# Kernel optimization log

Measured on AMD Instinct MI355X. Metric: run time of the kernel, lower is better.

Reference implementation:

```python
import jax, jax.numpy as jnp
import numpy as np

KERNEL = 3
DILATIONS = (2, 3)
NUM_HEADS = 8


def _unfold_windows(t, k, dil):
    # t: [B, C, H, W] -> [B, C, k*k, H, W], same layout as nn.Unfold(k, dil, pad=dil*(k-1)//2)
    B, C, H, W = t.shape
    pad = dil * (k - 1) // 2
    tp = jnp.pad(t, ((0, 0), (0, 0), (pad, pad), (pad, pad)))
    ws = [tp[:, :, i * dil:i * dil + H, j * dil:j * dil + W]
          for i in range(k) for j in range(k)]
    return jnp.stack(ws, axis=2)


def _dilate_attention(q, k_, v, kernel, dil, head_dim):
    # q,k_,v: [B, d, H, W]
    B, d, H, W = q.shape
    nh = d // head_dim
    scale = head_dim ** (-0.5)
    qh = q.reshape(B, nh, head_dim, H, W)
    kw = _unfold_windows(k_, kernel, dil).reshape(B, nh, head_dim, kernel * kernel, H, W)
    vw = _unfold_windows(v, kernel, dil).reshape(B, nh, head_dim, kernel * kernel, H, W)
    attn = jax.nn.softmax(jnp.einsum('bndhw,bndkhw->bnkhw', qh, kw) * scale, axis=2)
    out = jnp.einsum('bnkhw,bndkhw->bndhw', attn, vw)  # [B, nh, hd, H, W]
    return out.transpose(0, 3, 4, 1, 2).reshape(B, H, W, d)


def setup_inputs() -> dict:
    key = jax.random.key(0)
    k1, k2, k3, k4 = jax.random.split(key, 4)
    B, H, W, C = 4, 128, 128, 256
    x = jax.random.normal(k1, (B, H, W, C), dtype=jnp.float32)
    Wqkv = jax.random.normal(k2, (3 * C, C), dtype=jnp.float32) * (C ** -0.5)
    Wproj = jax.random.normal(k3, (C, C), dtype=jnp.float32) * (C ** -0.5)
    bproj = jnp.zeros((C,), dtype=jnp.float32)
    return {"x": x, "Wqkv": Wqkv, "Wproj": Wproj, "bproj": bproj}


def reference(x, Wqkv, Wproj, bproj):
    B, H, W, C = x.shape
    nd = len(DILATIONS)
    head_dim = C // NUM_HEADS
    # 1x1 conv qkv (no bias), then split into 3 and nd dilation groups
    qkv = jnp.einsum('bhwc,oc->bohw', x, Wqkv).reshape(B, 3, nd, C // nd, H, W)
    outs = []
    for i, dil in enumerate(DILATIONS):
        q, k_, v = qkv[:, 0, i], qkv[:, 1, i], qkv[:, 2, i]
        outs.append(_dilate_attention(q, k_, v, KERNEL, dil, head_dim))
    xo = jnp.concatenate(outs, axis=-1)  # [B, H, W, C], dilation-group-major channels
    return jnp.einsum('bhwc,oc->bhwo', xo, Wproj) + bproj
```

## Files before the change

kernel.cpp:

```cpp
#include <hip/hip_runtime.h>
#include <stdint.h>


typedef __attribute__((ext_vector_type(8))) short bf16x8;
typedef __attribute__((ext_vector_type(4))) float f32x4;
typedef __attribute__((ext_vector_type(2))) float f32x2;

__device__ __forceinline__ f32x2 up2(unsigned u) {
  union { unsigned u; float f; } a, b;
  a.u = u << 16;
  b.u = u & 0xffff0000u;
  return (f32x2){a.f, b.f};
}
__device__ __forceinline__ unsigned short f2bf(float f) {
  union { float f; unsigned u; } x; x.f = f;
  unsigned r = x.u + 0x7fffu + ((x.u >> 16) & 1u);
  return (unsigned short)(r >> 16);
}
__device__ __forceinline__ unsigned pk2bf(float a, float b) {
  return (unsigned)f2bf(a) | ((unsigned)f2bf(b) << 16);
}
__device__ __forceinline__ unsigned cvtpk(float a, float b) {
  unsigned r;
  asm("v_cvt_pk_bf16_f32 %0, %1, %2" : "=v"(r) : "v"(a), "v"(b));
  return r;
}

__global__ __launch_bounds__(256) void cvt_w_both(
    const float* __restrict__ wqkv, const float* __restrict__ wproj,
    unsigned short* __restrict__ dst) {
  const int i = (blockIdx.x * 256 + threadIdx.x) * 8;
  const float* src = (i < 196608) ? (wqkv + i) : (wproj + (i - 196608));
  const float4* s = (const float4*)src;
  float4 a = s[0], b = s[1];
  uint4 o;
  o.x = pk2bf(a.x, a.y); o.y = pk2bf(a.z, a.w);
  o.z = pk2bf(b.x, b.y); o.w = pk2bf(b.z, b.w);
  *(uint4*)(dst + i) = o;
}

#define BARX()                                                \
  do {                                                        \
    asm volatile("s_waitcnt lgkmcnt(0)" ::: "memory");        \
    __builtin_amdgcn_s_barrier();                             \
    __builtin_amdgcn_sched_barrier(0);                        \
  } while (0)
#define WAITVM(n)                                             \
  do {                                                        \
    asm volatile("s_waitcnt vmcnt(" #n ")" ::: "memory");     \
    __builtin_amdgcn_sched_barrier(0);                        \
  } while (0)

template <int OUTF32, int AF32>
__global__ __launch_bounds__(256) void gemm_bt(
    const void* __restrict__ Ap, const unsigned short* __restrict__ B,
    void* __restrict__ Cout, const float* __restrict__ bias,
    int N, int NT) {
  __shared__ __align__(16) unsigned short lds[24576];

  const int tid  = threadIdx.x;
  const int lane = tid & 63;
  const int wv   = tid >> 6;
  const int wr   = wv >> 1;
  const int wc   = wv & 1;

  const int nwg = gridDim.x;
  const int q8  = nwg >> 3;
  const int nid = (blockIdx.x & 7) * q8 + (blockIdx.x >> 3);
  const int n0  = (nid % NT) * 128;
  const int m0  = (nid / NT) * 128;

  const float* Af          = (const float*)Ap;
  const unsigned short* Ab = (const unsigned short*)Ap;

  const int stg_rowB = wv * 16 + (lane >> 2);
  const int stg_kB   = ((lane & 3) ^ ((lane >> 3) & 3)) * 8;
  const unsigned short* Bg   = B  + (size_t)(n0 + stg_rowB) * 256 + stg_kB;
  const unsigned short* Ag16 = Ab + (size_t)(m0 + stg_rowB) * 256 + stg_kB;

  const int stg_rowA32 = wv * 8 + (lane >> 3);
  const int stg_kA32   = ((lane & 7) ^ (lane >> 3)) * 4;
  const float* Ag32 = Af + (size_t)(m0 + stg_rowA32) * 256 + stg_kA32;

  f32x4 acc[4][4];
#pragma unroll
  for (int i = 0; i < 4; ++i)
#pragma unroll
    for (int j = 0; j < 4; ++j) acc[i][j] = (f32x4){0.f, 0.f, 0.f, 0.f};

  const int a_r = lane & 15;

#define STAGE16(buf, kt)                                                       \
  do {                                                                         \
    const unsigned short* Asrc = Ag16 + (kt) * 32;                             \
    const unsigned short* Bsrc = Bg + (kt) * 32;                               \
    _Pragma("unroll")                                                          \
    for (int it = 0; it < 2; ++it) {                                           \
      __builtin_amdgcn_global_load_lds(                                        \
          (const __attribute__((address_space(1))) void*)(Asrc + (size_t)it * 64 * 256), \
          (__attribute__((address_space(3))) void*)&lds[(buf) * 8192 + it * 2048 + wv * 512], \
          16, 0, 0);                                                           \
      __builtin_amdgcn_global_load_lds(                                        \
          (const __attribute__((address_space(1))) void*)(Bsrc + (size_t)it * 64 * 256), \
          (__attribute__((address_space(3))) void*)&lds[(buf) * 8192 + 4096 + it * 2048 + wv * 512], \
          16, 0, 0);                                                           \
    }                                                                          \
  } while (0)

#define COMPUTE16(buf)                                                         \
  do {                                                                         \
    const int gsw = (((lane >> 4) ^ ((lane >> 1) & 3))) * 8;                   \
    bf16x8 af[4], bfr[4];                                                      \
    _Pragma("unroll")                                                          \
    for (int mi = 0; mi < 4; ++mi)                                             \
      af[mi] = *(const bf16x8*)&lds[(buf) * 8192 + (wr * 64 + mi * 16 + a_r) * 32 + gsw]; \
    _Pragma("unroll")                                                          \
    for (int ni = 0; ni < 4; ++ni)                                             \
      bfr[ni] = *(const bf16x8*)&lds[(buf) * 8192 + 4096 + (wc * 64 + ni * 16 + a_r) * 32 + gsw]; \
    _Pragma("unroll")                                                          \
    for (int mi = 0; mi < 4; ++mi)                                             \
      _Pragma("unroll")                                                        \
      for (int ni = 0; ni < 4; ++ni)                                           \
        acc[mi][ni] = __builtin_amdgcn_mfma_f32_16x16x32_bf16(                 \
            af[mi], bfr[ni], acc[mi][ni], 0, 0, 0);                            \
  } while (0)

#define STAGE32(buf, kt)                                                       \
  do {                                                                         \
    const float* Asrc = Ag32 + (kt) * 32;                                      \
    const unsigned short* Bsrc = Bg + (kt) * 32;                               \
    _Pragma("unroll")                                                          \
    for (int it = 0; it < 4; ++it)                                             \
      __builtin_amdgcn_global_load_lds(                                        \
          (const __attribute__((address_space(1))) void*)(Asrc + (size_t)it * 32 * 256), \
          (__attribute__((address_space(3))) void*)&lds[(buf) * 12288 + it * 2048 + wv * 512], \
          16, 0, 0);                                                           \
    _Pragma("unroll")                                                          \
    for (int it = 0; it < 2; ++it)                                             \
      __builtin_amdgcn_global_load_lds(                                        \
          (const __attribute__((address_space(1))) void*)(Bsrc + (size_t)it * 64 * 256), \
          (__attribute__((address_space(3))) void*)&lds[(buf) * 12288 + 8192 + it * 2048 + wv * 512], \
          16, 0, 0);                                                           \
  } while (0)

#define COMPUTE32(buf)                                                         \
  do {                                                                         \
    const int gswB = (((lane >> 4) ^ ((lane >> 1) & 3))) * 8;                  \
    const int sA0  = ((2 * (lane >> 4)) ^ (lane & 7)) * 4;                     \
    const int sA1  = (((2 * (lane >> 4)) ^ (lane & 7)) ^ 1) * 4;               \
    const float* Afl = (const float*)lds;                                      \
    bf16x8 af[4], bfr[4];                                                      \
    _Pragma("unroll")                                                          \
    for (int mi = 0; mi < 4; ++mi) {                                           \
      const int rb = (buf) * 6144 + (wr * 64 + mi * 16 + a_r) * 32;            \
      f32x4 lo = *(const f32x4*)&Afl[rb + sA0];                                \
      f32x4 hi = *(const f32x4*)&Afl[rb + sA1];                                \
      uint4 pk;                                                                \
      pk.x = cvtpk(lo.x, lo.y); pk.y = cvtpk(lo.z, lo.w);                      \
      pk.z = cvtpk(hi.x, hi.y); pk.w = cvtpk(hi.z, hi.w);                      \
      af[mi] = *(bf16x8*)&pk;                                                  \
    }                                                                          \
    _Pragma("unroll")                                                          \
    for (int ni = 0; ni < 4; ++ni)                                             \
      bfr[ni] = *(const bf16x8*)&lds[(buf) * 12288 + 8192 + (wc * 64 + ni * 16 + a_r) * 32 + gswB]; \
    _Pragma("unroll")                                                          \
    for (int mi = 0; mi < 4; ++mi)                                             \
      _Pragma("unroll")                                                        \
      for (int ni = 0; ni < 4; ++ni)                                           \
        acc[mi][ni] = __builtin_amdgcn_mfma_f32_16x16x32_bf16(                 \
            af[mi], bfr[ni], acc[mi][ni], 0, 0, 0);                            \
  } while (0)

  if constexpr (AF32) {
    STAGE32(0, 0);
    STAGE32(1, 1);
    WAITVM(6);  BARX();
    COMPUTE32(0); BARX();
    STAGE32(0, 2); WAITVM(6); BARX();
    COMPUTE32(1); BARX();
    STAGE32(1, 3); WAITVM(6); BARX();
    COMPUTE32(0); BARX();
    STAGE32(0, 4); WAITVM(6); BARX();
    COMPUTE32(1); BARX();
    STAGE32(1, 5); WAITVM(6); BARX();
    COMPUTE32(0); BARX();
    STAGE32(0, 6); WAITVM(6); BARX();
    COMPUTE32(1); BARX();
    STAGE32(1, 7); WAITVM(6); BARX();
    COMPUTE32(0); BARX();
    WAITVM(0);   BARX();
    COMPUTE32(1); BARX();
  } else {
    STAGE16(0, 0);
    STAGE16(1, 1);
    WAITVM(4); BARX();
    COMPUTE16(0); STAGE16(2, 2); WAITVM(4); BARX();
    COMPUTE16(1); STAGE16(0, 3); WAITVM(4); BARX();
    COMPUTE16(2); STAGE16(1, 4); WAITVM(4); BARX();
    COMPUTE16(0); STAGE16(2, 5); WAITVM(4); BARX();
    COMPUTE16(1); STAGE16(0, 6); WAITVM(4); BARX();
    COMPUTE16(2); STAGE16(1, 7); WAITVM(4); BARX();
    COMPUTE16(0); WAITVM(0);   BARX();
    COMPUTE16(1); BARX();
  }

  const int cl = wc * 64 + a_r;
  const int rl = wr * 64 + (lane >> 4) * 4;
  if (!OUTF32) {
    unsigned short* eb = &lds[0];
#pragma unroll
    for (int ni = 0; ni < 4; ++ni)
#pragma unroll
      for (int mi = 0; mi < 4; ++mi)
#pragma unroll
        for (int r = 0; r < 4; ++r)
          eb[(rl + mi * 16 + r) * 136 + cl + ni * 16] = f2bf(acc[mi][ni][r]);
    BARX();
    unsigned short* C = (unsigned short*)Cout;
#pragma unroll
    for (int p = 0; p < 8; ++p) {
      const int idx = p * 256 + tid;
      const int row = idx >> 4;
      const int seg = idx & 15;
      uint4 v = *(const uint4*)&eb[row * 136 + seg * 8];
      *(uint4*)&C[(size_t)(m0 + row) * N + n0 + seg * 8] = v;
    }
  } else {
    float* ef = (float*)&lds[0];
    float* C = (float*)Cout;
    float bv[4];
#pragma unroll
    for (int ni = 0; ni < 4; ++ni) bv[ni] = bias[n0 + wc * 64 + ni * 16 + a_r];
#pragma unroll
    for (int half = 0; half < 2; ++half) {
      if (wr == half) {
        const int rb = (lane >> 4) * 4;
#pragma unroll
        for (int ni = 0; ni < 4; ++ni)
#pragma unroll
          for (int mi = 0; mi < 4; ++mi)
#pragma unroll
            for (int r = 0; r < 4; ++r)
              ef[(rb + mi * 16 + r) * 132 + wc * 64 + ni * 16 + a_r] =
                  acc[mi][ni][r] + bv[ni];
      }
      BARX();
#pragma unroll
      for (int p = 0; p < 8; ++p) {
        const int idx = p * 256 + tid;
        const int row = idx >> 5;
        const int seg = idx & 31;
        f32x4 v = *(const f32x4*)&ef[row * 132 + seg * 4];
        *(f32x4*)&C[(size_t)(m0 + half * 64 + row) * N + n0 + seg * 4] = v;
      }
      BARX();
    }
  }
#undef STAGE16
#undef COMPUTE16
#undef STAGE32
#undef COMPUTE32
}

__global__ __launch_bounds__(512) void attn_kernel(
    const unsigned short* __restrict__ qkv, unsigned short* __restrict__ xo) {
  __shared__ __align__(16) unsigned short lds[4 * 485 * 8];

  const int nwg = gridDim.x;
  const int q8  = nwg >> 3;
  const int nid = (blockIdx.x & 7) * q8 + (blockIdx.x >> 3);
  const int combo = nid & 7;
  const int tw    = (nid >> 3) & 7;
  const int th    = (nid >> 6) & 7;
  const int b     = nid >> 9;
  const int d     = (combo >> 2) ? 3 : 2;
  const int choff = combo * 32;
  const int h0 = th * 16, w0 = tw * 16;
  const int t = threadIdx.x;

  const int splane = t & 3;
  const int t4     = t >> 2;
  const int schoff = choff + splane * 8;

#pragma unroll
  for (int it = 0; it < 4; ++it) {
    const int px = it * 128 + t4;
    const int r = px / 22, c = px % 22;
    const int gh = h0 - d + r;
    const int gw = w0 - d + c;
    const bool ok = ((unsigned)gh < 128u) && ((unsigned)gw < 128u);
    const int hcl = min(max(gh, 0), 127);
    const int wcl = min(max(gw, 0), 127);
    const int gp = (((b << 7) | hcl) << 7) | wcl;
    uint4 u = *(const uint4*)(qkv + (size_t)gp * 768 + 256 + schoff);
    if (!ok) u = make_uint4(0u, 0u, 0u, 0u);
    if (it < 3 || t < 400) *(uint4*)&lds[(splane * 485 + px) * 8] = u;
  }

  const int half = t & 1;
  const int ph = (t >> 1) >> 4, pw = (t >> 1) & 15;
  const int gp0 = (((b << 7) | (h0 + ph)) << 7) | (w0 + pw);
  const unsigned short* qp = qkv + (size_t)gp0 * 768 + choff + half * 16;
  uint4 uq0 = *(const uint4*)qp;
  uint4 uq1 = *(const uint4*)(qp + 8);
  f32x2 q2[8];
  {
    const f32x2 s2 = {0.17677669529663687f, 0.17677669529663687f};
    q2[0] = up2(uq0.x) * s2; q2[1] = up2(uq0.y) * s2;
    q2[2] = up2(uq0.z) * s2; q2[3] = up2(uq0.w) * s2;
    q2[4] = up2(uq1.x) * s2; q2[5] = up2(uq1.y) * s2;
    q2[6] = up2(uq1.z) * s2; q2[7] = up2(uq1.w) * s2;
  }
  __syncthreads();

  const int p0 = 2 * half, p1 = 2 * half + 1;
  float sc[9];
#pragma unroll
  for (int i = 0; i < 3; ++i) {
#pragma unroll
    for (int j = 0; j < 3; ++j) {
      const int lp = (ph + i * d) * 22 + (pw + j * d);
      const uint4 k0 = *(const uint4*)&lds[(p0 * 485 + lp) * 8];
      const uint4 k1 = *(const uint4*)&lds[(p1 * 485 + lp) * 8];
      f32x2 a = q2[0] * up2(k0.x);
      a += q2[1] * up2(k0.y); a += q2[2] * up2(k0.z); a += q2[3] * up2(k0.w);
      a += q2[4] * up2(k1.x); a += q2[5] * up2(k1.y);
      a += q2[6] * up2(k1.z); a += q2[7] * up2(k1.w);
      sc[i * 3 + j] = a.x + a.y;
    }
  }
#pragma unroll
  for (int k = 0; k < 9; ++k) sc[k] += __shfl_xor(sc[k], 1);

  float mx = sc[0];
#pragma unroll
  for (int k = 1; k < 9; ++k) mx = fmaxf(mx, sc[k]);
  float sum = 0.f;
#pragma unroll
  for (int k = 0; k < 9; ++k) { sc[k] = __expf(sc[k] - mx); sum += sc[k]; }
  const float inv = 1.f / sum;

  __syncthreads();
#pragma unroll
  for (int it = 0; it < 4; ++it) {
    const int px = it * 128 + t4;
    const int r = px / 22, c = px % 22;
    const int gh = h0 - d + r;
    const int gw = w0 - d + c;
    const bool ok = ((unsigned)gh < 128u) && ((unsigned)gw < 128u);
    const int hcl = min(max(gh, 0), 127);
    const int wcl = min(max(gw, 0), 127);
    const int gp = (((b << 7) | hcl) << 7) | wcl;
    uint4 u = *(const uint4*)(qkv + (size_t)gp * 768 + 512 + schoff);
    if (!ok) u = make_uint4(0u, 0u, 0u, 0u);
    if (it < 3 || t < 400) *(uint4*)&lds[(splane * 485 + px) * 8] = u;
  }
  __syncthreads();

  f32x2 o2[8];
#pragma unroll
  for (int k = 0; k < 8; ++k) o2[k] = (f32x2){0.f, 0.f};
#pragma unroll
  for (int i = 0; i < 3; ++i) {
#pragma unroll
    for (int j = 0; j < 3; ++j) {
      const int lp = (ph + i * d) * 22 + (pw + j * d);
      const uint4 v0 = *(const uint4*)&lds[(p0 * 485 + lp) * 8];
      const uint4 v1 = *(const uint4*)&lds[(p1 * 485 + lp) * 8];
      const float wv = sc[i * 3 + j] * inv;
      const f32x2 w2 = {wv, wv};
      o2[0] += w2 * up2(v0.x); o2[1] += w2 * up2(v0.y);
      o2[2] += w2 * up2(v0.z); o2[3] += w2 * up2(v0.w);
      o2[4] += w2 * up2(v1.x); o2[5] += w2 * up2(v1.y);
      o2[6] += w2 * up2(v1.z); o2[7] += w2 * up2(v1.w);
    }
  }

  unsigned short* op = xo + (size_t)gp0 * 256 + choff + half * 16;
  uint4 s0, s1;
  s0.x = pk2bf(o2[0].x, o2[0].y); s0.y = pk2bf(o2[1].x, o2[1].y);
  s0.z = pk2bf(o2[2].x, o2[2].y); s0.w = pk2bf(o2[3].x, o2[3].y);
  s1.x = pk2bf(o2[4].x, o2[4].y); s1.y = pk2bf(o2[5].x, o2[5].y);
  s1.z = pk2bf(o2[6].x, o2[6].y); s1.w = pk2bf(o2[7].x, o2[7].y);
  *(uint4*)op       = s0;
  *(uint4*)(op + 8) = s1;
}

extern "C" void kernel_launch(void* const* d_in, const int* in_sizes, int n_in,
                              void* d_out, int out_size, void* d_ws, size_t ws_size,
                              hipStream_t stream) {
  const float* x     = (const float*)d_in[0];
  const float* Wqkv  = (const float*)d_in[1];
  const float* Wproj = (const float*)d_in[2];
  const float* bproj = (const float*)d_in[3];

  const int M = 4 * 128 * 128;
  const int C = 256;

  unsigned short* qkvb   = (unsigned short*)d_ws;
  unsigned short* xob    = qkvb + (size_t)M * 3 * C;
  unsigned short* wqkvb  = xob + (size_t)M * C;
  unsigned short* wprojb = wqkvb + (size_t)3 * C * C;
  (void)wprojb;

  cvt_w_both<<<128, 256, 0, stream>>>(Wqkv, Wproj, wqkvb);

  gemm_bt<0, 1><<<(M / 128) * (3 * C / 128), 256, 0, stream>>>(
      (const void*)x, wqkvb, (void*)qkvb, nullptr, 3 * C, 3 * C / 128);

  attn_kernel<<<2048, 512, 0, stream>>>(qkvb, xob);

  gemm_bt<1, 0><<<(M / 128) * (C / 128), 256, 0, stream>>>(
      (const void*)xob, wqkvb + (size_t)3 * C * C, d_out, bproj, C, C / 128);
}
```

Measured before the change: 110.7 us.

## Specialize projection GEMM to full-width 128x256 tiles with 512 threads

Splits the templated GEMM into a QKV kernel and a dedicated projection kernel. Each projection workgroup now covers all 256 output columns for 128 rows with 8 waves, so every A tile is loaded once instead of twice, and the projection drops from three-stage to two-stage buffering. This is meant to cut redundant global loads of the attention output and halve the number of projection workgroups. The trade-off is fewer, larger blocks with higher LDS use per block, less overlap from the shallower pipeline, and an epilogue that writes the fp32 result in four quarter passes.

```diff
diff --git a/kernel.cpp b/kernel.cpp
--- a/kernel.cpp
+++ b/kernel.cpp
@@ -51,11 +51,9 @@
     __builtin_amdgcn_sched_barrier(0);                        \
   } while (0)
 
-template <int OUTF32, int AF32>
-__global__ __launch_bounds__(256) void gemm_bt(
-    const void* __restrict__ Ap, const unsigned short* __restrict__ B,
-    void* __restrict__ Cout, const float* __restrict__ bias,
-    int N, int NT) {
+__global__ __launch_bounds__(256) void gemm_qkv(
+    const float* __restrict__ Af, const unsigned short* __restrict__ B,
+    unsigned short* __restrict__ Cout, int N, int NT) {
   __shared__ __align__(16) unsigned short lds[24576];
 
   const int tid  = threadIdx.x;
@@ -70,13 +68,9 @@
   const int n0  = (nid % NT) * 128;
   const int m0  = (nid / NT) * 128;
 
-  const float* Af          = (const float*)Ap;
-  const unsigned short* Ab = (const unsigned short*)Ap;
-
   const int stg_rowB = wv * 16 + (lane >> 2);
   const int stg_kB   = ((lane & 3) ^ ((lane >> 3) & 3)) * 8;
-  const unsigned short* Bg   = B  + (size_t)(n0 + stg_rowB) * 256 + stg_kB;
-  const unsigned short* Ag16 = Ab + (size_t)(m0 + stg_rowB) * 256 + stg_kB;
+  const unsigned short* Bg = B + (size_t)(n0 + stg_rowB) * 256 + stg_kB;
 
   const int stg_rowA32 = wv * 8 + (lane >> 3);
   const int stg_kA32   = ((lane & 7) ^ (lane >> 3)) * 4;
@@ -89,41 +83,6 @@
     for (int j = 0; j < 4; ++j) acc[i][j] = (f32x4){0.f, 0.f, 0.f, 0.f};
 
   const int a_r = lane & 15;
-
-#define STAGE16(buf, kt)                                                       \
-  do {                                                                         \
-    const unsigned short* Asrc = Ag16 + (kt) * 32;                             \
-    const unsigned short* Bsrc = Bg + (kt) * 32;                               \
-    _Pragma("unroll")                                                          \
-    for (int it = 0; it < 2; ++it) {                                           \
-      __builtin_amdgcn_global_load_lds(                                        \
-          (const __attribute__((address_space(1))) void*)(Asrc + (size_t)it * 64 * 256), \
-          (__attribute__((address_space(3))) void*)&lds[(buf) * 8192 + it * 2048 + wv * 512], \
-          16, 0, 0);                                                           \
-      __builtin_amdgcn_global_load_lds(                                        \
-          (const __attribute__((address_space(1))) void*)(Bsrc + (size_t)it * 64 * 256), \
-          (__attribute__((address_space(3))) void*)&lds[(buf) * 8192 + 4096 + it * 2048 + wv * 512], \
-          16, 0, 0);                                                           \
-    }                                                                          \
-  } while (0)
-
-#define COMPUTE16(buf)                                                         \
-  do {                                                                         \
-    const int gsw = (((lane >> 4) ^ ((lane >> 1) & 3))) * 8;                   \
-    bf16x8 af[4], bfr[4];                                                      \
-    _Pragma("unroll")                                                          \
-    for (int mi = 0; mi < 4; ++mi)                                             \
-      af[mi] = *(const bf16x8*)&lds[(buf) * 8192 + (wr * 64 + mi * 16 + a_r) * 32 + gsw]; \
-    _Pragma("unroll")                                                          \
-    for (int ni = 0; ni < 4; ++ni)                                             \
-      bfr[ni] = *(const bf16x8*)&lds[(buf) * 8192 + 4096 + (wc * 64 + ni * 16 + a_r) * 32 + gsw]; \
-    _Pragma("unroll")                                                          \
-    for (int mi = 0; mi < 4; ++mi)                                             \
-      _Pragma("unroll")                                                        \
-      for (int ni = 0; ni < 4; ++ni)                                           \
-        acc[mi][ni] = __builtin_amdgcn_mfma_f32_16x16x32_bf16(                 \
-            af[mi], bfr[ni], acc[mi][ni], 0, 0, 0);                            \
-  } while (0)
 
 #define STAGE32(buf, kt)                                                       \
   do {                                                                         \
@@ -171,95 +130,160 @@
             af[mi], bfr[ni], acc[mi][ni], 0, 0, 0);                            \
   } while (0)
 
-  if constexpr (AF32) {
-    STAGE32(0, 0);
-    STAGE32(1, 1);
-    WAITVM(6);  BARX();
-    COMPUTE32(0); BARX();
-    STAGE32(0, 2); WAITVM(6); BARX();
-    COMPUTE32(1); BARX();
-    STAGE32(1, 3); WAITVM(6); BARX();
-    COMPUTE32(0); BARX();
-    STAGE32(0, 4); WAITVM(6); BARX();
-    COMPUTE32(1); BARX();
-    STAGE32(1, 5); WAITVM(6); BARX();
-    COMPUTE32(0); BARX();
-    STAGE32(0, 6); WAITVM(6); BARX();
-    COMPUTE32(1); BARX();
-    STAGE32(1, 7); WAITVM(6); BARX();
-    COMPUTE32(0); BARX();
-    WAITVM(0);   BARX();
-    COMPUTE32(1); BARX();
-  } else {
-    STAGE16(0, 0);
-    STAGE16(1, 1);
-    WAITVM(4); BARX();
-    COMPUTE16(0); STAGE16(2, 2); WAITVM(4); BARX();
-    COMPUTE16(1); STAGE16(0, 3); WAITVM(4); BARX();
-    COMPUTE16(2); STAGE16(1, 4); WAITVM(4); BARX();
-    COMPUTE16(0); STAGE16(2, 5); WAITVM(4); BARX();
-    COMPUTE16(1); STAGE16(0, 6); WAITVM(4); BARX();
-    COMPUTE16(2); STAGE16(1, 7); WAITVM(4); BARX();
-    COMPUTE16(0); WAITVM(0);   BARX();
-    COMPUTE16(1); BARX();
-  }
+  STAGE32(0, 0);
+  STAGE32(1, 1);
+  WAITVM(6);  BARX();
+  COMPUTE32(0); BARX();
+  STAGE32(0, 2); WAITVM(6); BARX();
+  COMPUTE32(1); BARX();
+  STAGE32(1, 3); WAITVM(6); BARX();
+  COMPUTE32(0); BARX();
+  STAGE32(0, 4); WAITVM(6); BARX();
+  COMPUTE32(1); BARX();
+  STAGE32(1, 5); WAITVM(6); BARX();
+  COMPUTE32(0); BARX();
+  STAGE32(0, 6); WAITVM(6); BARX();
+  COMPUTE32(1); BARX();
+  STAGE32(1, 7); WAITVM(6); BARX();
+  COMPUTE32(0); BARX();
+  WAITVM(0);   BARX();
+  COMPUTE32(1); BARX();
 
   const int cl = wc * 64 + a_r;
   const int rl = wr * 64 + (lane >> 4) * 4;
-  if (!OUTF32) {
-    unsigned short* eb = &lds[0];
-#pragma unroll
-    for (int ni = 0; ni < 4; ++ni)
-#pragma unroll
-      for (int mi = 0; mi < 4; ++mi)
-#pragma unroll
-        for (int r = 0; r < 4; ++r)
-          eb[(rl + mi * 16 + r) * 136 + cl + ni * 16] = f2bf(acc[mi][ni][r]);
-    BARX();
-    unsigned short* C = (unsigned short*)Cout;
-#pragma unroll
-    for (int p = 0; p < 8; ++p) {
-      const int idx = p * 256 + tid;
-      const int row = idx >> 4;
-      const int seg = idx & 15;
-      uint4 v = *(const uint4*)&eb[row * 136 + seg * 8];
-      *(uint4*)&C[(size_t)(m0 + row) * N + n0 + seg * 8] = v;
-    }
-  } else {
-    float* ef = (float*)&lds[0];
-    float* C = (float*)Cout;
-    float bv[4];
-#pragma unroll
-    for (int ni = 0; ni < 4; ++ni) bv[ni] = bias[n0 + wc * 64 + ni * 16 + a_r];
-#pragma unroll
-    for (int half = 0; half < 2; ++half) {
-      if (wr == half) {
-        const int rb = (lane >> 4) * 4;
-#pragma unroll
-        for (int ni = 0; ni < 4; ++ni)
-#pragma unroll
-          for (int mi = 0; mi < 4; ++mi)
-#pragma unroll
-            for (int r = 0; r < 4; ++r)
-              ef[(rb + mi * 16 + r) * 132 + wc * 64 + ni * 16 + a_r] =
-                  acc[mi][ni][r] + bv[ni];
-      }
-      BARX();
-#pragma unroll
-      for (int p = 0; p < 8; ++p) {
-        const int idx = p * 256 + tid;
-        const int row = idx >> 5;
-        const int seg = idx & 31;
-        f32x4 v = *(const f32x4*)&ef[row * 132 + seg * 4];
-        *(f32x4*)&C[(size_t)(m0 + half * 64 + row) * N + n0 + seg * 4] = v;
-      }
-      BARX();
-    }
-  }
-#undef STAGE16
-#undef COMPUTE16
+  unsigned short* eb = &lds[0];
+#pragma unroll
+  for (int ni = 0; ni < 4; ++ni)
+#pragma unroll
+    for (int mi = 0; mi < 4; ++mi)
+#pragma unroll
+      for (int r = 0; r < 4; ++r)
+        eb[(rl + mi * 16 + r) * 136 + cl + ni * 16] = f2bf(acc[mi][ni][r]);
+  BARX();
+#pragma unroll
+  for (int p = 0; p < 8; ++p) {
+    const int idx = p * 256 + tid;
+    const int row = idx >> 4;
+    const int seg = idx & 15;
+    uint4 v = *(const uint4*)&eb[row * 136 + seg * 8];
+    *(uint4*)&Cout[(size_t)(m0 + row) * N + n0 + seg * 8] = v;
+  }
 #undef STAGE32
 #undef COMPUTE32
+}
+
+__global__ __launch_bounds__(512) void gemm_proj(
+    const unsigned short* __restrict__ A, const unsigned short* __restrict__ B,
+    float* __restrict__ C, const float* __restrict__ bias) {
+  __shared__ __align__(16) unsigned short lds[24576];
+
+  const int tid  = threadIdx.x;
+  const int lane = tid & 63;
+  const int wv   = tid >> 6;
+  const int wr   = wv >> 2;
+  const int wc   = wv & 3;
+
+  const int nwg = gridDim.x;
+  const int q8  = nwg >> 3;
+  const int nid = (blockIdx.x & 7) * q8 + (blockIdx.x >> 3);
+  const int m0  = nid * 128;
+
+  const int stg_row = tid >> 2;
+  const int stg_k   = ((tid & 3) ^ ((tid >> 3) & 3)) * 8;
+  const unsigned short* Ag = A + (size_t)(m0 + stg_row) * 256 + stg_k;
+  const unsigned short* Bg = B + (size_t)stg_row * 256 + stg_k;
+
+  f32x4 acc[4][4];
+#pragma unroll
+  for (int i = 0; i < 4; ++i)
+#pragma unroll
+    for (int j = 0; j < 4; ++j) acc[i][j] = (f32x4){0.f, 0.f, 0.f, 0.f};
+
+  const int a_r = lane & 15;
+
+#define PSTAGE(buf, kt)                                                        \
+  do {                                                                         \
+    __builtin_amdgcn_global_load_lds(                                          \
+        (const __attribute__((address_space(1))) void*)(Ag + (kt) * 32),       \
+        (__attribute__((address_space(3))) void*)&lds[(buf) * 12288 + wv * 512], \
+        16, 0, 0);                                                             \
+    _Pragma("unroll")                                                          \
+    for (int it = 0; it < 2; ++it)                                             \
+      __builtin_amdgcn_global_load_lds(                                        \
+          (const __attribute__((address_space(1))) void*)(Bg + (size_t)it * 128 * 256 + (kt) * 32), \
+          (__attribute__((address_space(3))) void*)&lds[(buf) * 12288 + 4096 + it * 4096 + wv * 512], \
+          16, 0, 0);                                                           \
+  } while (0)
+
+#define PCOMPUTE(buf)                                                          \
+  do {                                                                         \
+    const int gsw = (((lane >> 4) ^ ((lane >> 1) & 3))) * 8;                   \
+    bf16x8 af[4], bfr[4];                                                      \
+    _Pragma("unroll")                                                          \
+    for (int mi = 0; mi < 4; ++mi)                                             \
+      af[mi] = *(const bf16x8*)&lds[(buf) * 12288 + (wr * 64 + mi * 16 + a_r) * 32 + gsw]; \
+    _Pragma("unroll")                                                          \
+    for (int ni = 0; ni < 4; ++ni)                                             \
+      bfr[ni] = *(const bf16x8*)&lds[(buf) * 12288 + 4096 + (wc * 64 + ni * 16 + a_r) * 32 + gsw]; \
+    _Pragma("unroll")                                                          \
+    for (int mi = 0; mi < 4; ++mi)                                             \
+      _Pragma("unroll")                                                        \
+      for (int ni = 0; ni < 4; ++ni)                                           \
+        acc[mi][ni] = __builtin_amdgcn_mfma_f32_16x16x32_bf16(                 \
+            af[mi], bfr[ni], acc[mi][ni], 0, 0, 0);                            \
+  } while (0)
+
+  PSTAGE(0, 0);
+  PSTAGE(1, 1);
+  WAITVM(3);  BARX();
+  PCOMPUTE(0); BARX();
+  PSTAGE(0, 2); WAITVM(3); BARX();
+  PCOMPUTE(1); BARX();
+  PSTAGE(1, 3); WAITVM(3); BARX();
+  PCOMPUTE(0); BARX();
+  PSTAGE(0, 4); WAITVM(3); BARX();
+  PCOMPUTE(1); BARX();
+  PSTAGE(1, 5); WAITVM(3); BARX();
+  PCOMPUTE(0); BARX();
+  PSTAGE(0, 6); WAITVM(3); BARX();
+  PCOMPUTE(1); BARX();
+  PSTAGE(1, 7); WAITVM(3); BARX();
+  PCOMPUTE(0); BARX();
+  WAITVM(0);   BARX();
+  PCOMPUTE(1); BARX();
+
+  float bv[4];
+#pragma unroll
+  for (int ni = 0; ni < 4; ++ni) bv[ni] = bias[wc * 64 + ni * 16 + a_r];
+  float* ef = (float*)&lds[0];
+#pragma unroll
+  for (int q = 0; q < 4; ++q) {
+    if (wr == (q >> 1)) {
+      const int mlo = 2 * (q & 1);
+#pragma unroll
+      for (int mi2 = 0; mi2 < 2; ++mi2) {
+        const int mi = mlo + mi2;
+#pragma unroll
+        for (int ni = 0; ni < 4; ++ni)
+#pragma unroll
+          for (int r = 0; r < 4; ++r)
+            ef[((lane >> 4) * 4 + mi2 * 16 + r) * 264 + wc * 64 + ni * 16 + a_r] =
+                acc[mi][ni][r] + bv[ni];
+      }
+    }
+    BARX();
+#pragma unroll
+    for (int p = 0; p < 4; ++p) {
+      const int idx = p * 512 + tid;
+      const int row = idx >> 6;
+      const int seg = idx & 63;
+      f32x4 v = *(const f32x4*)&ef[row * 264 + seg * 4];
+      *(f32x4*)&C[(size_t)(m0 + q * 32 + row) * 256 + seg * 4] = v;
+    }
+    BARX();
+  }
+#undef PSTAGE
+#undef PCOMPUTE
 }
 
 __global__ __launch_bounds__(512) void attn_kernel(
@@ -401,15 +425,13 @@
   unsigned short* xob    = qkvb + (size_t)M * 3 * C;
   unsigned short* wqkvb  = xob + (size_t)M * C;
   unsigned short* wprojb = wqkvb + (size_t)3 * C * C;
-  (void)wprojb;
 
   cvt_w_both<<<128, 256, 0, stream>>>(Wqkv, Wproj, wqkvb);
 
-  gemm_bt<0, 1><<<(M / 128) * (3 * C / 128), 256, 0, stream>>>(
-      (const void*)x, wqkvb, (void*)qkvb, nullptr, 3 * C, 3 * C / 128);
+  gemm_qkv<<<(M / 128) * (3 * C / 128), 256, 0, stream>>>(
+      x, wqkvb, qkvb, 3 * C, 3 * C / 128);
 
   attn_kernel<<<2048, 512, 0, stream>>>(qkvb, xob);
 
-  gemm_bt<1, 0><<<(M / 128) * (C / 128), 256, 0, stream>>>(
-      (const void*)xob, wqkvb + (size_t)3 * C * C, d_out, bproj, C, C / 128);
-}
+  gemm_proj<<<M / 128, 512, 0, stream>>>(xob, wprojb, (float*)d_out, bproj);
+}
```

Result: slower. 113.7 us (+2.7%).
